# Kernel tuning notes

Hardware: AMD Instinct MI355X
Metric: run time of the kernel (lower is better)

Reference implementation:

```python
import jax, jax.numpy as jnp
import numpy as np

B, SQ, SK, H, DH = 4, 4096, 462, 10, 64  # batch, img tokens, text tokens, heads, head dim


def setup_inputs() -> dict:
    key = jax.random.key(0)
    k1, k2, k3, k4, k5 = jax.random.split(key, 5)
    q = jax.random.normal(k1, (B, SQ, H * DH), dtype=jnp.float32)
    k = jax.random.normal(k2, (B, SK, H * DH), dtype=jnp.float32)
    v = jax.random.normal(k3, (B, SK, H * DH), dtype=jnp.float32)
    # mask_scale = H*W / sum(mask) in the original -> positive, >= 1
    mask_scale = 1.0 + 3.0 * jax.random.uniform(k4, (B, H, SQ, SK), dtype=jnp.float32)
    mask_bool = jax.random.randint(k5, (B, H, SQ, SK), 0, 2).astype(bool)
    # guarantee every query row attends to at least one key (avoid all -inf rows)
    mask_bool = mask_bool.at[..., 0].set(True)
    return {"q": q, "k": k, "v": v, "mask_bool": mask_bool,
            "mask_scale": mask_scale, "heads": H}


def reference(q, k, v, mask_bool, mask_scale, heads):
    b, sq, d = q.shape
    dh = d // heads
    # [b, s, h*dh] -> [b, h, s, dh]
    qh = q.reshape(b, sq, heads, dh).transpose(0, 2, 1, 3)
    kh = k.reshape(b, -1, heads, dh).transpose(0, 2, 1, 3)
    vh = v.reshape(b, -1, heads, dh).transpose(0, 2, 1, 3)
    scale = 1.0 / np.sqrt(dh).astype(np.float32)
    scores = jnp.einsum("bhqd,bhkd->bhqk", qh, kh) * scale
    scores = scores * mask_scale
    scores = jnp.where(mask_bool, scores, -jnp.inf)
    attn = jax.nn.softmax(scores, axis=-1)
    out = jnp.einsum("bhqk,bhkd->bhqd", attn, vh)
    return out.transpose(0, 2, 1, 3).reshape(b, sq, d)
```

## Files before the change

kernel.cpp:

```cpp
#include <hip/hip_runtime.h>

#define B_  4
#define SQ_ 4096
#define SK_ 462
#define H_  10
#define DH_ 64
#define D_  (H_ * DH_)
#define SKP_ 480
#define KT_  15

typedef _Float16 half8 __attribute__((ext_vector_type(8)));
typedef float floatx4 __attribute__((ext_vector_type(4)));

#define K16_ELEMS ((size_t)B_ * H_ * SKP_ * DH_)
#define WS_NEEDED (2 * K16_ELEMS * sizeof(_Float16))

__device__ int g_mask_fmt;

__global__ void detect_mask_fmt(const unsigned int* __restrict__ mb_dw) {
  __shared__ int s_float, s_byte;
  if (threadIdx.x == 0) { s_float = 0; s_byte = 0; }
  __syncthreads();
  int fl = 0, by = 0;
  for (int i = threadIdx.x; i < 1024; i += 256) {
    unsigned int x = mb_dw[i];
    if (x > 1u) {
      if (x == 0x3F800000u) fl = 1; else by = 1;
    }
  }
  if (fl) atomicOr(&s_float, 1);
  if (by) atomicOr(&s_byte, 1);
  __syncthreads();
  if (threadIdx.x == 0) g_mask_fmt = s_float ? 2 : (s_byte ? 1 : 0);
}

__device__ __forceinline__ half8 cvt8(float4 a, float4 b) {
  half8 o;
  o[0] = (_Float16)a.x; o[1] = (_Float16)a.y;
  o[2] = (_Float16)a.z; o[3] = (_Float16)a.w;
  o[4] = (_Float16)b.x; o[5] = (_Float16)b.y;
  o[6] = (_Float16)b.z; o[7] = (_Float16)b.w;
  return o;
}

__global__ void convert_kv(const float* __restrict__ k, const float* __restrict__ v,
                           _Float16* __restrict__ k16, _Float16* __restrict__ vt16) {
  int t = blockIdx.x * 256 + threadIdx.x;
  const int NK = B_ * H_ * SKP_ * (DH_ / 8);
  const int NV = B_ * H_ * DH_ * (SKP_ / 8);
  if (t < NK) {
    int d8  = t & 7;
    int key = (t >> 3) % SKP_;
    int bh  = t / (8 * SKP_);
    int b = bh / H_, h = bh % H_;
    half8 o;
    if (key < SK_) {
      const float* src = k + ((size_t)(b * SK_ + key)) * D_ + h * DH_ + d8 * 8;
      float4 f0 = *reinterpret_cast<const float4*>(src);
      float4 f1 = *reinterpret_cast<const float4*>(src + 4);
      o = cvt8(f0, f1);
    } else {
      #pragma unroll
      for (int j = 0; j < 8; ++j) o[j] = (_Float16)0.0f;
    }
    *reinterpret_cast<half8*>(k16 + ((size_t)bh * SKP_ + key) * DH_ + d8 * 8) = o;
  } else if (t < NK + NV) {
    int u  = t - NK;
    int k8 = u % (SKP_ / 8);
    int d  = (u / (SKP_ / 8)) % DH_;
    int bh = u / ((SKP_ / 8) * DH_);
    int b = bh / H_, h = bh % H_;
    half8 o;
    #pragma unroll
    for (int j = 0; j < 8; ++j) {
      int key = k8 * 8 + j;
      o[j] = (key < SK_)
               ? (_Float16)v[((size_t)(b * SK_ + key)) * D_ + h * DH_ + d]
               : (_Float16)0.0f;
    }
    *reinterpret_cast<half8*>(vt16 + ((size_t)bh * DH_ + d) * SKP_ + k8 * 8) = o;
  }
}

template<bool WS, bool MBYTE>
__device__ __forceinline__ void attn_body(
    const float* __restrict__ q, const float* __restrict__ k,
    const float* __restrict__ v, const void* __restrict__ mb,
    const float* __restrict__ msc, float* __restrict__ out,
    const _Float16* __restrict__ k16, const _Float16* __restrict__ vt16,
    _Float16 (&ps)[4][16][34]) {
  const int tid  = threadIdx.x;
  const int wave = tid >> 6;
  const int lane = tid & 63;
  const int l16  = lane & 15;
  const int g4   = lane >> 4;

  const int b  = blockIdx.z;
  const int h  = blockIdx.y;
  const int q0 = blockIdx.x * 64;
  const int bh = b * H_ + h;

  half8 aq[2];
  {
    const float* qp = q + ((size_t)(b * SQ_ + q0 + wave * 16 + l16)) * D_ + h * DH_;
    #pragma unroll
    for (int kk = 0; kk < 2; ++kk) {
      float4 f0 = *reinterpret_cast<const float4*>(qp + kk * 32 + g4 * 8);
      float4 f1 = *reinterpret_cast<const float4*>(qp + kk * 32 + g4 * 8 + 4);
      aq[kk] = cvt8(f0, f1);
    }
  }

  floatx4 o_acc[4];
  floatx4 l_acc;
  #pragma unroll
  for (int nt = 0; nt < 4; ++nt)
    #pragma unroll
    for (int r = 0; r < 4; ++r) o_acc[nt][r] = 0.0f;
  #pragma unroll
  for (int r = 0; r < 4; ++r) l_acc[r] = 0.0f;
  float m2[4] = {-1e30f, -1e30f, -1e30f, -1e30f};

  unsigned int rowoff[4];
  #pragma unroll
  for (int r = 0; r < 4; ++r) {
    int qrow = q0 + wave * 16 + g4 * 4 + r;
    rowoff[r] = (unsigned int)((b * H_ + h) * SQ_ + qrow) * SK_;
  }

  half8 ones_f;
  #pragma unroll
  for (int j = 0; j < 8; ++j) ones_f[j] = (_Float16)1.0f;

  const float c2 = 0.18033688011112042f;

  const unsigned char* mbb = (const unsigned char*)mb;
  const unsigned int*  mbd = (const unsigned int*)mb;

  auto load_masks = [&](int kt_, float (&m_)[2][4]) {
    #pragma unroll
    for (int ct = 0; ct < 2; ++ct)
      #pragma unroll
      for (int r = 0; r < 4; ++r) {
        int col = kt_ * 32 + ct * 16 + l16;
        int cc  = col < SK_ ? col : SK_ - 1;
        unsigned int idx = rowoff[r] + (unsigned int)cc;
        float sc = msc[idx];
        unsigned int mvv = MBYTE ? (unsigned int)mbb[idx] : mbd[idx];
        m_[ct][r] = (mvv != 0u && col < SK_) ? sc : 0.0f;
      }
  };

  float mC[2][4];
  load_masks(0, mC);

  const _Float16* kbase16 = k16 + (size_t)bh * SKP_ * DH_;
  const _Float16* vbase16 = vt16 + (size_t)bh * DH_ * SKP_;
  const float* kbase = k + (size_t)(b * SK_) * D_ + h * DH_;
  const float* vbase = v + (size_t)(b * SK_) * D_ + h * DH_;

  for (int kt = 0; kt < KT_; ++kt) {
    half8 kbf[2][2];
    if constexpr (WS) {
      const _Float16* kp = kbase16 + (size_t)(kt * 32) * DH_;
      #pragma unroll
      for (int ct = 0; ct < 2; ++ct)
        #pragma unroll
        for (int kk = 0; kk < 2; ++kk)
          kbf[ct][kk] = *reinterpret_cast<const half8*>(
              kp + (ct * 16 + l16) * DH_ + kk * 32 + g4 * 8);
    } else {
      #pragma unroll
      for (int ct = 0; ct < 2; ++ct) {
        int key = kt * 32 + ct * 16 + l16;
        int kc  = key < SK_ ? key : SK_ - 1;
        #pragma unroll
        for (int kk = 0; kk < 2; ++kk) {
          const float* kp = kbase + (size_t)kc * D_ + kk * 32 + g4 * 8;
          float4 f0 = *reinterpret_cast<const float4*>(kp);
          float4 f1 = *reinterpret_cast<const float4*>(kp + 4);
          kbf[ct][kk] = cvt8(f0, f1);
        }
      }
    }

    half8 vbf[4];
    if constexpr (WS) {
      const _Float16* vp = vbase16 + kt * 32 + g4 * 8;
      #pragma unroll
      for (int nt = 0; nt < 4; ++nt)
        vbf[nt] = *reinterpret_cast<const half8*>(vp + (size_t)(nt * 16 + l16) * SKP_);
    } else {
      #pragma unroll
      for (int nt = 0; nt < 4; ++nt) {
        int dim = nt * 16 + l16;
        #pragma unroll
        for (int j = 0; j < 8; ++j) {
          int key = kt * 32 + g4 * 8 + j;
          vbf[nt][j] = (key < SK_)
                         ? (_Float16)vbase[(size_t)key * D_ + dim]
                         : (_Float16)0.0f;
        }
      }
    }

    float mN[2][4];
    if (kt + 1 < KT_) load_masks(kt + 1, mN);

    floatx4 s[2];
    #pragma unroll
    for (int ct = 0; ct < 2; ++ct)
      #pragma unroll
      for (int r = 0; r < 4; ++r) s[ct][r] = 0.0f;
    #pragma unroll
    for (int ct = 0; ct < 2; ++ct)
      #pragma unroll
      for (int kk = 0; kk < 2; ++kk)
        s[ct] = __builtin_amdgcn_mfma_f32_16x16x32_f16(aq[kk], kbf[ct][kk], s[ct], 0, 0, 0);

    float pw[2][4];
    #pragma unroll
    for (int r = 0; r < 4; ++r) {
      float sc0 = mC[0][r], sc1 = mC[1][r];
      float s0 = (sc0 != 0.0f) ? s[0][r] * (c2 * sc0) : -1e30f;
      float s1 = (sc1 != 0.0f) ? s[1][r] * (c2 * sc1) : -1e30f;
      float mx = fmaxf(s0, s1);
      mx = fmaxf(mx, __shfl_xor(mx, 1));
      mx = fmaxf(mx, __shfl_xor(mx, 2));
      mx = fmaxf(mx, __shfl_xor(mx, 4));
      mx = fmaxf(mx, __shfl_xor(mx, 8));
      float mnew  = fmaxf(m2[r], mx);
      float alpha = exp2f(m2[r] - mnew);
      m2[r] = mnew;
      pw[0][r] = exp2f(s0 - mnew);
      pw[1][r] = exp2f(s1 - mnew);
      l_acc[r] *= alpha;
      #pragma unroll
      for (int nt = 0; nt < 4; ++nt) o_acc[nt][r] *= alpha;
    }

    #pragma unroll
    for (int ct = 0; ct < 2; ++ct)
      #pragma unroll
      for (int r = 0; r < 4; ++r)
        ps[wave][g4 * 4 + r][ct * 16 + l16] = (_Float16)pw[ct][r];
    asm volatile("s_waitcnt lgkmcnt(0)" ::: "memory");
    half8 pa;
    #pragma unroll
    for (int j = 0; j < 8; ++j) pa[j] = ps[wave][l16][g4 * 8 + j];

    #pragma unroll
    for (int nt = 0; nt < 4; ++nt)
      o_acc[nt] = __builtin_amdgcn_mfma_f32_16x16x32_f16(pa, vbf[nt], o_acc[nt], 0, 0, 0);
    l_acc = __builtin_amdgcn_mfma_f32_16x16x32_f16(pa, ones_f, l_acc, 0, 0, 0);

    if (kt + 1 < KT_) {
      #pragma unroll
      for (int ct = 0; ct < 2; ++ct)
        #pragma unroll
        for (int r = 0; r < 4; ++r) mC[ct][r] = mN[ct][r];
    }
  }

  #pragma unroll
  for (int r = 0; r < 4; ++r) {
    float inv = 1.0f / l_acc[r];
    int qrow = q0 + wave * 16 + g4 * 4 + r;
    float* ob = out + (size_t)(b * SQ_ + qrow) * D_ + h * DH_;
    #pragma unroll
    for (int nt = 0; nt < 4; ++nt)
      ob[nt * 16 + l16] = o_acc[nt][r] * inv;
  }
}

template<bool WS>
__global__ __launch_bounds__(256, 3)
void attn_fwd(const float* __restrict__ q, const float* __restrict__ k,
              const float* __restrict__ v, const void* __restrict__ mb,
              const float* __restrict__ msc, float* __restrict__ out,
              const _Float16* __restrict__ k16, const _Float16* __restrict__ vt16) {
  __shared__ __align__(16) _Float16 ps[4][16][34];
  if (g_mask_fmt == 1) attn_body<WS, true >(q, k, v, mb, msc, out, k16, vt16, ps);
  else                 attn_body<WS, false>(q, k, v, mb, msc, out, k16, vt16, ps);
}

extern "C" void kernel_launch(void* const* d_in, const int* in_sizes, int n_in,
                              void* d_out, int out_size, void* d_ws, size_t ws_size,
                              hipStream_t stream) {
  const float* q   = (const float*)d_in[0];
  const float* k   = (const float*)d_in[1];
  const float* v   = (const float*)d_in[2];
  const void*  mb  = d_in[3];
  const float* msc = (const float*)d_in[4];
  float* out = (float*)d_out;

  detect_mask_fmt<<<1, 256, 0, stream>>>((const unsigned int*)mb);

  _Float16* k16  = (_Float16*)d_ws;
  _Float16* vt16 = k16 + K16_ELEMS;

  dim3 grid(SQ_ / 64, H_, B_);
  if (d_ws != nullptr && ws_size >= WS_NEEDED) {
    convert_kv<<<1200, 256, 0, stream>>>(k, v, k16, vt16);
    attn_fwd<true><<<grid, 256, 0, stream>>>(q, k, v, mb, msc, out, k16, vt16);
  } else {
    attn_fwd<false><<<grid, 256, 0, stream>>>(q, k, v, mb, msc, out, k16, vt16);
  }
}
```

Baseline: 833.5 us.

## Pre-pack boolean mask into bitfields and stage mask_scale tiles via coalesced LDS loads

Adds a pre-pass kernel that uses wave ballots to compress the boolean mask into 16 dwords of bits per query row. A new attention kernel reads those bits once into LDS and loads mask_scale as coalesced float2 rows two tiles ahead, staged through shared memory, instead of strided scalar loads per element. This aims to cut mask-related global traffic and latency in the bandwidth-bound attention loop. The cost is an extra kernel pass over the full mask, more workspace and more LDS per block.

```diff
diff --git a/kernel.cpp b/kernel.cpp
--- a/kernel.cpp
+++ b/kernel.cpp
@@ -8,12 +8,16 @@
 #define D_  (H_ * DH_)
 #define SKP_ 480
 #define KT_  15
+#define MBDW_ 16
 
 typedef _Float16 half8 __attribute__((ext_vector_type(8)));
 typedef float floatx4 __attribute__((ext_vector_type(4)));
+typedef float float2v __attribute__((ext_vector_type(2)));
 
 #define K16_ELEMS ((size_t)B_ * H_ * SKP_ * DH_)
-#define WS_NEEDED (2 * K16_ELEMS * sizeof(_Float16))
+#define MBITS_DW  ((size_t)B_ * H_ * SQ_ * MBDW_)
+#define WS_KV     (2 * K16_ELEMS * sizeof(_Float16))
+#define WS_FULL   (WS_KV + MBITS_DW * 4)
 
 __device__ int g_mask_fmt;
 
@@ -82,13 +86,37 @@
   }
 }
 
-template<bool WS, bool MBYTE>
-__device__ __forceinline__ void attn_body(
-    const float* __restrict__ q, const float* __restrict__ k,
-    const float* __restrict__ v, const void* __restrict__ mb,
-    const float* __restrict__ msc, float* __restrict__ out,
-    const _Float16* __restrict__ k16, const _Float16* __restrict__ vt16,
-    _Float16 (&ps)[4][16][34]) {
+__global__ __launch_bounds__(256)
+void build_mbits(const void* __restrict__ mb, unsigned int* __restrict__ mbits) {
+  const int fmt  = g_mask_fmt;
+  const int lane = threadIdx.x & 63;
+  const int wgid = (blockIdx.x * 256 + threadIdx.x) >> 6;
+  const unsigned char* mbb = (const unsigned char*)mb;
+  const unsigned int*  mbd = (const unsigned int*)mb;
+  for (int rr = 0; rr < 16; ++rr) {
+    int row = wgid * 16 + rr;
+    size_t rb = (size_t)row * SK_;
+    #pragma unroll
+    for (int i = 0; i < 8; ++i) {
+      int col = i * 64 + lane;
+      int mv = 0;
+      if (col < SK_) mv = (fmt == 1) ? (mbb[rb + col] != 0) : (mbd[rb + col] != 0u);
+      unsigned long long bal = __ballot(mv);
+      if (lane == 0)  mbits[(size_t)row * MBDW_ + i * 2]     = (unsigned int)bal;
+      if (lane == 32) mbits[(size_t)row * MBDW_ + i * 2 + 1] = (unsigned int)(bal >> 32);
+    }
+  }
+}
+
+__global__ __launch_bounds__(256, 4)
+void attn_fwd_full(const float* __restrict__ q, const float* __restrict__ msc,
+                   float* __restrict__ out,
+                   const _Float16* __restrict__ k16, const _Float16* __restrict__ vt16,
+                   const unsigned int* __restrict__ mbits) {
+  __shared__ __align__(16) _Float16     ps[4][16][34];
+  __shared__ __align__(16) float        ms[4][16][34];
+  __shared__ __align__(16) unsigned int mbl[4][16][16];
+
   const int tid  = threadIdx.x;
   const int wave = tid >> 6;
   const int lane = tid & 63;
@@ -111,6 +139,13 @@
     }
   }
 
+  {
+    int i = lane >> 2, c4 = (lane & 3) * 4;
+    size_t row = (size_t)bh * SQ_ + (q0 + wave * 16 + i);
+    uint4 w = *reinterpret_cast<const uint4*>(mbits + row * MBDW_ + c4);
+    *reinterpret_cast<uint4*>(&mbl[wave][i][c4]) = w;
+  }
+
   floatx4 o_acc[4];
   floatx4 l_acc;
   #pragma unroll
@@ -121,47 +156,46 @@
   for (int r = 0; r < 4; ++r) l_acc[r] = 0.0f;
   float m2[4] = {-1e30f, -1e30f, -1e30f, -1e30f};
 
-  unsigned int rowoff[4];
-  #pragma unroll
-  for (int r = 0; r < 4; ++r) {
-    int qrow = q0 + wave * 16 + g4 * 4 + r;
-    rowoff[r] = (unsigned int)((b * H_ + h) * SQ_ + qrow) * SK_;
-  }
-
   half8 ones_f;
   #pragma unroll
   for (int j = 0; j < 8; ++j) ones_f[j] = (_Float16)1.0f;
 
   const float c2 = 0.18033688011112042f;
 
-  const unsigned char* mbb = (const unsigned char*)mb;
-  const unsigned int*  mbd = (const unsigned int*)mb;
-
-  auto load_masks = [&](int kt_, float (&m_)[2][4]) {
-    #pragma unroll
-    for (int ct = 0; ct < 2; ++ct)
-      #pragma unroll
-      for (int r = 0; r < 4; ++r) {
-        int col = kt_ * 32 + ct * 16 + l16;
-        int cc  = col < SK_ ? col : SK_ - 1;
-        unsigned int idx = rowoff[r] + (unsigned int)cc;
-        float sc = msc[idx];
-        unsigned int mvv = MBYTE ? (unsigned int)mbb[idx] : mbd[idx];
-        m_[ct][r] = (mvv != 0u && col < SK_) ? sc : 0.0f;
-      }
+  const size_t mrow = ((size_t)bh * SQ_ + (q0 + wave * 16 + (lane >> 2))) * SK_;
+  float2v rA[4], rB[4];
+  auto issue_msc = [&](int kt_, float2v (&rg)[4]) {
+    #pragma unroll
+    for (int p = 0; p < 4; ++p) {
+      int c = kt_ * 32 + ((lane & 3) + p * 4) * 2;
+      c = (c <= SK_ - 2) ? c : (SK_ - 2);
+      rg[p] = *reinterpret_cast<const float2v*>(msc + mrow + c);
+    }
   };
-
-  float mC[2][4];
-  load_masks(0, mC);
+  auto write_tile = [&](float2v (&rg)[4]) {
+    int i = lane >> 2;
+    #pragma unroll
+    for (int p = 0; p < 4; ++p) {
+      int c = ((lane & 3) + p * 4) * 2;
+      *reinterpret_cast<float2v*>(&ms[wave][i][c]) = rg[p];
+    }
+  };
+
+  issue_msc(0, rA);
+  issue_msc(1, rB);
+  write_tile(rA);
+  #pragma unroll
+  for (int p = 0; p < 4; ++p) rA[p] = rB[p];
 
   const _Float16* kbase16 = k16 + (size_t)bh * SKP_ * DH_;
   const _Float16* vbase16 = vt16 + (size_t)bh * DH_ * SKP_;
-  const float* kbase = k + (size_t)(b * SK_) * D_ + h * DH_;
-  const float* vbase = v + (size_t)(b * SK_) * D_ + h * DH_;
 
   for (int kt = 0; kt < KT_; ++kt) {
+    if (kt + 2 < KT_) issue_msc(kt + 2, rB);
+    __builtin_amdgcn_sched_barrier(0);
+
     half8 kbf[2][2];
-    if constexpr (WS) {
+    {
       const _Float16* kp = kbase16 + (size_t)(kt * 32) * DH_;
       #pragma unroll
       for (int ct = 0; ct < 2; ++ct)
@@ -169,43 +203,14 @@
         for (int kk = 0; kk < 2; ++kk)
           kbf[ct][kk] = *reinterpret_cast<const half8*>(
               kp + (ct * 16 + l16) * DH_ + kk * 32 + g4 * 8);
-    } else {
-      #pragma unroll
-      for (int ct = 0; ct < 2; ++ct) {
-        int key = kt * 32 + ct * 16 + l16;
-        int kc  = key < SK_ ? key : SK_ - 1;
-        #pragma unroll
-        for (int kk = 0; kk < 2; ++kk) {
-          const float* kp = kbase + (size_t)kc * D_ + kk * 32 + g4 * 8;
-          float4 f0 = *reinterpret_cast<const float4*>(kp);
-          float4 f1 = *reinterpret_cast<const float4*>(kp + 4);
-          kbf[ct][kk] = cvt8(f0, f1);
-        }
-      }
-    }
-
+    }
     half8 vbf[4];
-    if constexpr (WS) {
+    {
       const _Float16* vp = vbase16 + kt * 32 + g4 * 8;
       #pragma unroll
       for (int nt = 0; nt < 4; ++nt)
         vbf[nt] = *reinterpret_cast<const half8*>(vp + (size_t)(nt * 16 + l16) * SKP_);
-    } else {
-      #pragma unroll
-      for (int nt = 0; nt < 4; ++nt) {
-        int dim = nt * 16 + l16;
-        #pragma unroll
-        for (int j = 0; j < 8; ++j) {
-          int key = kt * 32 + g4 * 8 + j;
-          vbf[nt][j] = (key < SK_)
-                         ? (_Float16)vbase[(size_t)key * D_ + dim]
-                         : (_Float16)0.0f;
-        }
-      }
-    }
-
-    float mN[2][4];
-    if (kt + 1 < KT_) load_masks(kt + 1, mN);
+    }
 
     floatx4 s[2];
     #pragma unroll
@@ -217,6 +222,16 @@
       #pragma unroll
       for (int kk = 0; kk < 2; ++kk)
         s[ct] = __builtin_amdgcn_mfma_f32_16x16x32_f16(aq[kk], kbf[ct][kk], s[ct], 0, 0, 0);
+
+    float mC[2][4];
+    #pragma unroll
+    for (int r = 0; r < 4; ++r) {
+      unsigned int mw = mbl[wave][g4 * 4 + r][kt];
+      float v0 = ms[wave][g4 * 4 + r][l16];
+      float v1 = ms[wave][g4 * 4 + r][16 + l16];
+      mC[0][r] = ((mw >> l16) & 1u)        ? v0 : 0.0f;
+      mC[1][r] = ((mw >> (16 + l16)) & 1u) ? v1 : 0.0f;
+    }
 
     float pw[2][4];
     #pragma unroll
@@ -255,6 +270,193 @@
     l_acc = __builtin_amdgcn_mfma_f32_16x16x32_f16(pa, ones_f, l_acc, 0, 0, 0);
 
     if (kt + 1 < KT_) {
+      write_tile(rA);
+      #pragma unroll
+      for (int p = 0; p < 4; ++p) rA[p] = rB[p];
+    }
+  }
+
+  #pragma unroll
+  for (int r = 0; r < 4; ++r) {
+    float inv = 1.0f / l_acc[r];
+    int qrow = q0 + wave * 16 + g4 * 4 + r;
+    float* ob = out + (size_t)(b * SQ_ + qrow) * D_ + h * DH_;
+    #pragma unroll
+    for (int nt = 0; nt < 4; ++nt)
+      ob[nt * 16 + l16] = o_acc[nt][r] * inv;
+  }
+}
+
+template<bool WS, bool MBYTE>
+__device__ __forceinline__ void attn_body(
+    const float* __restrict__ q, const float* __restrict__ k,
+    const float* __restrict__ v, const void* __restrict__ mb,
+    const float* __restrict__ msc, float* __restrict__ out,
+    const _Float16* __restrict__ k16, const _Float16* __restrict__ vt16,
+    _Float16 (&ps)[4][16][34]) {
+  const int tid  = threadIdx.x;
+  const int wave = tid >> 6;
+  const int lane = tid & 63;
+  const int l16  = lane & 15;
+  const int g4   = lane >> 4;
+  const int b  = blockIdx.z;
+  const int h  = blockIdx.y;
+  const int q0 = blockIdx.x * 64;
+  const int bh = b * H_ + h;
+
+  half8 aq[2];
+  {
+    const float* qp = q + ((size_t)(b * SQ_ + q0 + wave * 16 + l16)) * D_ + h * DH_;
+    #pragma unroll
+    for (int kk = 0; kk < 2; ++kk) {
+      float4 f0 = *reinterpret_cast<const float4*>(qp + kk * 32 + g4 * 8);
+      float4 f1 = *reinterpret_cast<const float4*>(qp + kk * 32 + g4 * 8 + 4);
+      aq[kk] = cvt8(f0, f1);
+    }
+  }
+
+  floatx4 o_acc[4];
+  floatx4 l_acc;
+  #pragma unroll
+  for (int nt = 0; nt < 4; ++nt)
+    #pragma unroll
+    for (int r = 0; r < 4; ++r) o_acc[nt][r] = 0.0f;
+  #pragma unroll
+  for (int r = 0; r < 4; ++r) l_acc[r] = 0.0f;
+  float m2[4] = {-1e30f, -1e30f, -1e30f, -1e30f};
+
+  unsigned int rowoff[4];
+  #pragma unroll
+  for (int r = 0; r < 4; ++r) {
+    int qrow = q0 + wave * 16 + g4 * 4 + r;
+    rowoff[r] = (unsigned int)((b * H_ + h) * SQ_ + qrow) * SK_;
+  }
+
+  half8 ones_f;
+  #pragma unroll
+  for (int j = 0; j < 8; ++j) ones_f[j] = (_Float16)1.0f;
+  const float c2 = 0.18033688011112042f;
+
+  const unsigned char* mbb = (const unsigned char*)mb;
+  const unsigned int*  mbd = (const unsigned int*)mb;
+
+  auto load_masks = [&](int kt_, float (&m_)[2][4]) {
+    #pragma unroll
+    for (int ct = 0; ct < 2; ++ct)
+      #pragma unroll
+      for (int r = 0; r < 4; ++r) {
+        int col = kt_ * 32 + ct * 16 + l16;
+        int cc  = col < SK_ ? col : SK_ - 1;
+        unsigned int idx = rowoff[r] + (unsigned int)cc;
+        float sc = msc[idx];
+        unsigned int mvv = MBYTE ? (unsigned int)mbb[idx] : mbd[idx];
+        m_[ct][r] = (mvv != 0u && col < SK_) ? sc : 0.0f;
+      }
+  };
+
+  float mC[2][4];
+  load_masks(0, mC);
+
+  const _Float16* kbase16 = k16 + (size_t)bh * SKP_ * DH_;
+  const _Float16* vbase16 = vt16 + (size_t)bh * DH_ * SKP_;
+  const float* kbase = k + (size_t)(b * SK_) * D_ + h * DH_;
+  const float* vbase = v + (size_t)(b * SK_) * D_ + h * DH_;
+
+  for (int kt = 0; kt < KT_; ++kt) {
+    half8 kbf[2][2];
+    if constexpr (WS) {
+      const _Float16* kp = kbase16 + (size_t)(kt * 32) * DH_;
+      #pragma unroll
+      for (int ct = 0; ct < 2; ++ct)
+        #pragma unroll
+        for (int kk = 0; kk < 2; ++kk)
+          kbf[ct][kk] = *reinterpret_cast<const half8*>(
+              kp + (ct * 16 + l16) * DH_ + kk * 32 + g4 * 8);
+    } else {
+      #pragma unroll
+      for (int ct = 0; ct < 2; ++ct) {
+        int key = kt * 32 + ct * 16 + l16;
+        int kc  = key < SK_ ? key : SK_ - 1;
+        #pragma unroll
+        for (int kk = 0; kk < 2; ++kk) {
+          const float* kp = kbase + (size_t)kc * D_ + kk * 32 + g4 * 8;
+          float4 f0 = *reinterpret_cast<const float4*>(kp);
+          float4 f1 = *reinterpret_cast<const float4*>(kp + 4);
+          kbf[ct][kk] = cvt8(f0, f1);
+        }
+      }
+    }
+    half8 vbf[4];
+    if constexpr (WS) {
+      const _Float16* vp = vbase16 + kt * 32 + g4 * 8;
+      #pragma unroll
+      for (int nt = 0; nt < 4; ++nt)
+        vbf[nt] = *reinterpret_cast<const half8*>(vp + (size_t)(nt * 16 + l16) * SKP_);
+    } else {
+      #pragma unroll
+      for (int nt = 0; nt < 4; ++nt) {
+        int dim = nt * 16 + l16;
+        #pragma unroll
+        for (int j = 0; j < 8; ++j) {
+          int key = kt * 32 + g4 * 8 + j;
+          vbf[nt][j] = (key < SK_)
+                         ? (_Float16)vbase[(size_t)key * D_ + dim]
+                         : (_Float16)0.0f;
+        }
+      }
+    }
+
+    float mN[2][4];
+    if (kt + 1 < KT_) load_masks(kt + 1, mN);
+
+    floatx4 s[2];
+    #pragma unroll
+    for (int ct = 0; ct < 2; ++ct)
+      #pragma unroll
+      for (int r = 0; r < 4; ++r) s[ct][r] = 0.0f;
+    #pragma unroll
+    for (int ct = 0; ct < 2; ++ct)
+      #pragma unroll
+      for (int kk = 0; kk < 2; ++kk)
+        s[ct] = __builtin_amdgcn_mfma_f32_16x16x32_f16(aq[kk], kbf[ct][kk], s[ct], 0, 0, 0);
+
+    float pw[2][4];
+    #pragma unroll
+    for (int r = 0; r < 4; ++r) {
+      float sc0 = mC[0][r], sc1 = mC[1][r];
+      float s0 = (sc0 != 0.0f) ? s[0][r] * (c2 * sc0) : -1e30f;
+      float s1 = (sc1 != 0.0f) ? s[1][r] * (c2 * sc1) : -1e30f;
+      float mx = fmaxf(s0, s1);
+      mx = fmaxf(mx, __shfl_xor(mx, 1));
+      mx = fmaxf(mx, __shfl_xor(mx, 2));
+      mx = fmaxf(mx, __shfl_xor(mx, 4));
+      mx = fmaxf(mx, __shfl_xor(mx, 8));
+      float mnew  = fmaxf(m2[r], mx);
+      float alpha = exp2f(m2[r] - mnew);
+      m2[r] = mnew;
+      pw[0][r] = exp2f(s0 - mnew);
+      pw[1][r] = exp2f(s1 - mnew);
+      l_acc[r] *= alpha;
+      #pragma unroll
+      for (int nt = 0; nt < 4; ++nt) o_acc[nt][r] *= alpha;
+    }
+
+    #pragma unroll
+    for (int ct = 0; ct < 2; ++ct)
+      #pragma unroll
+      for (int r = 0; r < 4; ++r)
+        ps[wave][g4 * 4 + r][ct * 16 + l16] = (_Float16)pw[ct][r];
+    asm volatile("s_waitcnt lgkmcnt(0)" ::: "memory");
+    half8 pa;
+    #pragma unroll
+    for (int j = 0; j < 8; ++j) pa[j] = ps[wave][l16][g4 * 8 + j];
+
+    #pragma unroll
+    for (int nt = 0; nt < 4; ++nt)
+      o_acc[nt] = __builtin_amdgcn_mfma_f32_16x16x32_f16(pa, vbf[nt], o_acc[nt], 0, 0, 0);
+    l_acc = __builtin_amdgcn_mfma_f32_16x16x32_f16(pa, ones_f, l_acc, 0, 0, 0);
+
+    if (kt + 1 < KT_) {
       #pragma unroll
       for (int ct = 0; ct < 2; ++ct)
         #pragma unroll
@@ -298,9 +500,14 @@
 
   _Float16* k16  = (_Float16*)d_ws;
   _Float16* vt16 = k16 + K16_ELEMS;
+  unsigned int* mbits = (unsigned int*)(vt16 + K16_ELEMS);
 
   dim3 grid(SQ_ / 64, H_, B_);
-  if (d_ws != nullptr && ws_size >= WS_NEEDED) {
+  if (d_ws != nullptr && ws_size >= WS_FULL) {
+    convert_kv<<<1200, 256, 0, stream>>>(k, v, k16, vt16);
+    build_mbits<<<2560, 256, 0, stream>>>(mb, mbits);
+    attn_fwd_full<<<grid, 256, 0, stream>>>(q, msc, out, k16, vt16, mbits);
+  } else if (d_ws != nullptr && ws_size >= WS_KV) {
     convert_kv<<<1200, 256, 0, stream>>>(k, v, k16, vt16);
     attn_fwd<true><<<grid, 256, 0, stream>>>(q, k, v, mb, msc, out, k16, vt16);
   } else {
```

Result: no change. 822.2 us (-1.4%).
